# Performance work log

Hardware: AMD Instinct MI355X
Metric: run time of the kernel (lower is better)

Reference implementation:

```python
import jax, jax.numpy as jnp
import numpy as np
from jax import lax

STRIDE = (1, 1, 1, 1)
PADDING = (1, 1, 1, 1)
DILATION = (1, 1, 1, 1)


def setup_inputs() -> dict:
    key = jax.random.key(0)
    k1, k2, k3 = jax.random.split(key, 3)
    x = jax.random.normal(k1, (4, 32, 8, 24, 24, 24), dtype=jnp.float32)
    # weight layout matches torch ConvTranspose: (C_in, C_out, l_k, d_k, h_k, w_k)
    weight = jax.random.normal(k2, (32, 32, 3, 3, 3, 3), dtype=jnp.float32) * 0.05
    bias = jax.random.normal(k3, (32,), dtype=jnp.float32) * 0.05
    return {"x": x, "weight": weight, "bias": bias}


def _conv_transpose_4d(x, weight):
    # Transposed conv == conv with lhs dilated by stride, kernel spatially
    # flipped, and padding d*(k-1) - p on each side of each spatial dim.
    # Output size per dim: (i-1)*s - 2p + d*(k-1) + 1, identical to the
    # torch module's looped ConvTranspose3d + temporal scatter-add.
    ksp = weight.shape[2:]
    pads = [(d * (k - 1) - p, d * (k - 1) - p)
            for k, p, d in zip(ksp, PADDING, DILATION)]
    w = jnp.flip(weight, axis=(2, 3, 4, 5))  # (C_in, C_out, l, d, h, w)
    return lax.conv_general_dilated(
        x, w,
        window_strides=(1, 1, 1, 1),
        padding=pads,
        lhs_dilation=STRIDE,
        rhs_dilation=DILATION,
        dimension_numbers=("NCLDHW", "IOLDHW", "NCLDHW"),
    )


def reference(x, weight, bias):
    out = _conv_transpose_4d(x, weight)
    return out + bias.reshape(1, -1, 1, 1, 1, 1)
```

## Files before the change

### kernel.cpp

```cpp
#include <hip/hip_runtime.h>

#define NN 4
#define CC 32
#define LL 8
#define DD 24
#define HH 24
#define WW 24

typedef short  bf16x8  __attribute__((ext_vector_type(8)));
typedef float  f32x16  __attribute__((ext_vector_type(16)));
typedef unsigned short ushort8 __attribute__((ext_vector_type(8)));

#define XP_CHUNKS 2249728
#define XP_ELEMS  (XP_CHUNKS * 8)
#define AG_ELEMS  82944

__device__ __forceinline__ unsigned short f2bf(float f) {
    union { float f; unsigned u; } v; v.f = f;
    unsigned r = v.u + 0x7FFFu + ((v.u >> 16) & 1u);
    return (unsigned short)(r >> 16);
}

__device__ __forceinline__ void gload16(const void* g, void* l) {
    __builtin_amdgcn_global_load_lds(
        (const __attribute__((address_space(1))) unsigned int*)g,
        (__attribute__((address_space(3))) unsigned int*)l, 16, 0, 0);
}

__global__ __launch_bounds__(256) void prep(const float* __restrict__ x,
                                            const float* __restrict__ wgt,
                                            unsigned short* __restrict__ xp,
                                            unsigned short* __restrict__ Ag) {
    const int id = blockIdx.x * 256 + threadIdx.x;
    if (id < XP_CHUNKS) {
        const int wp = id % 26;
        const int r  = id / 26;
        const int g  = r & 1;
        const int r2 = r >> 1;
        const int hp = r2 % 26;
        const int slab = r2 / 26;
        const int dp = slab % 26;
        const int s2 = slab / 26;
        const int l  = s2 & 7;
        const int n  = (s2 >> 3) & 3;
        const int cig = s2 >> 5;
        const int dx = dp - 1, hx = hp - 1, wx = wp - 1;
        ushort8 v = {0, 0, 0, 0, 0, 0, 0, 0};
        if ((unsigned)dx < DD && (unsigned)hx < HH && (unsigned)wx < WW) {
            const int ci0 = cig * 16 + g * 8;
            const float* src = x + ((((size_t)n * CC + ci0) * LL + l) * DD + dx) * (HH * WW)
                             + hx * WW + wx;
#pragma unroll
            for (int ci = 0; ci < 8; ++ci)
                v[ci] = f2bf(src[(size_t)ci * (LL * DD * HH * WW)]);
        }
        const size_t dstc = ((size_t)r2 * 26 + wp) * 2 + g;
        *reinterpret_cast<ushort8*>(xp + dstc * 8) = v;
    } else {
        const int i = id - XP_CHUNKS;
        if (i < AG_ELEMS) {
            const int j  = i & 7;
            const int ln = (i >> 3) & 63;
            const int rest = i >> 9;
            const int s  = rest % 9;
            const int r  = rest / 9;
            const int qd = r % 3;
            const int ql = (r / 3) % 3;
            const int cig = r / 9;
            const int co = ln & 31, gg = ln >> 5;
            const int ci = cig * 16 + gg * 8 + j;
            const int tap = ql * 27 + qd * 9 + s;
            Ag[i] = f2bf(wgt[((size_t)ci * CC + co) * 81 + 80 - tap]);
        }
    }
}

__global__ __launch_bounds__(384, 3) void convt4d_main(
    const unsigned short* __restrict__ xp, const unsigned short* __restrict__ Ag,
    const float* __restrict__ bias, float* __restrict__ out)
{
    __shared__ __align__(16) unsigned short xs[2][1378 * 8];
    __shared__ __align__(16) unsigned short As[2][576 * 8];

    int bid = (int)blockIdx.x;
    bid = (bid & 7) * 96 + (bid >> 3);
    const int n = bid / (LL * DD);
    const int l = (bid / DD) % LL;
    const int d = bid % DD;

    const int t    = (int)threadIdx.x;
    const int lane = t & 63;
    const int wave = t >> 6;
    const int g    = lane >> 5;
    const int dh   = (lane >> 3) & 3;
    const int dw   = lane & 7;
    const int h0   = wave * 4;

    const int ql0 = (l == 0) ? 1 : 0;
    const int nql = 3 - (l == 0) - (l == 7);
    const int nst = 6 * nql;

    f32x16 acc[3];
#pragma unroll
    for (int i = 0; i < 3; ++i)
#pragma unroll
        for (int j = 0; j < 16; ++j) acc[i][j] = 0.f;

    const int eb = ((h0 + dh) * 53 + dw * 2 + g) * 8;

    auto issue = [&](int st, int buf) {
        const int qd  = st % 3;
        const int r   = st / 3;
        const int ql  = ql0 + r % nql;
        const int cig = r / nql;
        const int lx  = l + ql - 1;
        const unsigned short* base =
            xp + (size_t)((((cig * 4 + n) * 8 + lx) * 26) + (d + qd)) * (676 * 16);
        unsigned short* dst = xs[buf];
#pragma unroll
        for (int k = 0; k < 4; ++k) {
            const int v = t + k * 384;
            if (k < 3 || v < 1378) {
                int row = v / 53;
                int su  = v - row;
                if (su > 1351) su = 1351;
                gload16(base + (size_t)su * 8, (char*)dst + (size_t)v * 16);
            }
        }
        const unsigned short* asrc = Ag + (size_t)((cig * 9 + ql * 3 + qd)) * 4608;
        gload16(asrc + (size_t)t * 8, (char*)As[buf] + (size_t)t * 16);
        if (t < 192)
            gload16(asrc + (size_t)(t + 384) * 8, (char*)As[buf] + (size_t)(t + 384) * 16);
    };

    issue(0, 0);

#pragma unroll 1
    for (int st = 0; st < nst; ++st) {
        const int buf = st & 1;
        __syncthreads();
        if (st + 1 < nst) issue(st + 1, buf ^ 1);

        const unsigned short* xb = xs[buf] + eb;
#pragma unroll
        for (int s = 0; s < 9; ++s) {
            bf16x8 a = *reinterpret_cast<const bf16x8*>(&As[buf][(s * 64 + lane) * 8]);
            const int qh = s / 3, qw = s % 3;
            const int o = (qh * 53 + qw * 2) * 8;
#pragma unroll
            for (int nt = 0; nt < 3; ++nt) {
                bf16x8 b = *reinterpret_cast<const bf16x8*>(xb + o + nt * 128);
                acc[nt] = __builtin_amdgcn_mfma_f32_32x32x16_bf16(a, b, acc[nt], 0, 0, 0);
            }
        }
    }

#pragma unroll
    for (int r = 0; r < 16; ++r) {
        const int co = (r & 3) + 8 * (r >> 2) + 4 * g;
        const float bv = bias[co];
        size_t ob = (((((size_t)n * CC + co) * LL + l) * DD + d) * HH + (h0 + dh)) * WW + dw;
        out[ob]      = acc[0][r] + bv;
        out[ob + 8]  = acc[1][r] + bv;
        out[ob + 16] = acc[2][r] + bv;
    }
}

extern "C" void kernel_launch(void* const* d_in, const int* in_sizes, int n_in,
                              void* d_out, int out_size, void* d_ws, size_t ws_size,
                              hipStream_t stream) {
    const float* x    = (const float*)d_in[0];
    const float* wgt  = (const float*)d_in[1];
    const float* bias = (const float*)d_in[2];
    float* out = (float*)d_out;

    unsigned short* xp = (unsigned short*)d_ws;
    unsigned short* Ag = xp + XP_ELEMS;

    prep<<<(XP_CHUNKS + AG_ELEMS) / 256, 256, 0, stream>>>(x, wgt, xp, Ag);
    convt4d_main<<<NN * LL * DD, 384, 0, stream>>>(xp, Ag, bias, out);
}
```

Before: 113.8 us.

## Compute two output depth slices per block to reuse input planes across qd taps

Each block now produces two adjacent d outputs over half the h range, with 192 threads. Every loaded input depth plane feeds both outputs' accumulators, which cuts redundant x-plane loads from three per output to two. Weights move to a triple-buffered ring keyed by tap. This doubles accumulator registers and drops the occupancy hint, which risks fewer resident waves and more complex scheduling.

```diff
diff --git a/kernel.cpp b/kernel.cpp
--- a/kernel.cpp
+++ b/kernel.cpp
@@ -75,18 +75,23 @@
     }
 }
 
-__global__ __launch_bounds__(384, 3) void convt4d_main(
+__global__ __launch_bounds__(192) void convt4d_main(
     const unsigned short* __restrict__ xp, const unsigned short* __restrict__ Ag,
     const float* __restrict__ bias, float* __restrict__ out)
 {
-    __shared__ __align__(16) unsigned short xs[2][1378 * 8];
-    __shared__ __align__(16) unsigned short As[2][576 * 8];
+    __shared__ __align__(16) unsigned short xs[2][742 * 8];
+    __shared__ __align__(16) unsigned short As[3][576 * 8];
 
     int bid = (int)blockIdx.x;
     bid = (bid & 7) * 96 + (bid >> 3);
-    const int n = bid / (LL * DD);
-    const int l = (bid / DD) % LL;
-    const int d = bid % DD;
+    const int hh = bid & 1;
+    const int r0 = bid >> 1;
+    const int pd = r0 % 12;
+    const int r1 = r0 / 12;
+    const int l  = r1 & 7;
+    const int n  = r1 >> 3;
+    const int d0 = pd * 2;
+    const int hb = hh * 12;
 
     const int t    = (int)threadIdx.x;
     const int lane = t & 63;
@@ -94,63 +99,111 @@
     const int g    = lane >> 5;
     const int dh   = (lane >> 3) & 3;
     const int dw   = lane & 7;
-    const int h0   = wave * 4;
 
     const int ql0 = (l == 0) ? 1 : 0;
     const int nql = 3 - (l == 0) - (l == 7);
-    const int nst = 6 * nql;
-
-    f32x16 acc[3];
-#pragma unroll
-    for (int i = 0; i < 3; ++i)
-#pragma unroll
-        for (int j = 0; j < 16; ++j) acc[i][j] = 0.f;
-
-    const int eb = ((h0 + dh) * 53 + dw * 2 + g) * 8;
-
-    auto issue = [&](int st, int buf) {
-        const int qd  = st % 3;
-        const int r   = st / 3;
+    const int nst = 8 * nql;
+    const int nq  = 6 * nql;
+
+    f32x16 acc[2][3];
+#pragma unroll
+    for (int o = 0; o < 2; ++o)
+#pragma unroll
+        for (int i = 0; i < 3; ++i)
+#pragma unroll
+            for (int j = 0; j < 16; ++j) acc[o][i][j] = 0.f;
+
+    const int eb = ((wave * 4 + dh) * 53 + dw * 2 + g) * 8;
+
+    auto issueX = [&](int st, int buf) {
+        const int p   = st & 3;
+        const int r   = st >> 2;
         const int ql  = ql0 + r % nql;
         const int cig = r / nql;
         const int lx  = l + ql - 1;
-        const unsigned short* base =
-            xp + (size_t)((((cig * 4 + n) * 8 + lx) * 26) + (d + qd)) * (676 * 16);
+        const int dpad = d0 + p;
+        const size_t base = ((size_t)(((cig * 4 + n) * 8 + lx) * 26) + dpad) * 1352
+                          + (size_t)hb * 52;
         unsigned short* dst = xs[buf];
 #pragma unroll
         for (int k = 0; k < 4; ++k) {
-            const int v = t + k * 384;
-            if (k < 3 || v < 1378) {
+            const int v = t + k * 192;
+            if (k < 3 || v < 742) {
                 int row = v / 53;
                 int su  = v - row;
-                if (su > 1351) su = 1351;
-                gload16(base + (size_t)su * 8, (char*)dst + (size_t)v * 16);
-            }
-        }
-        const unsigned short* asrc = Ag + (size_t)((cig * 9 + ql * 3 + qd)) * 4608;
-        gload16(asrc + (size_t)t * 8, (char*)As[buf] + (size_t)t * 16);
-        if (t < 192)
-            gload16(asrc + (size_t)(t + 384) * 8, (char*)As[buf] + (size_t)(t + 384) * 16);
+                if (su > 727) su = 727;
+                gload16(xp + (base + su) * 8, (char*)dst + (size_t)v * 16);
+            }
+        }
     };
-
-    issue(0, 0);
+    auto issueA = [&](int q) {
+        const int grp = q / 3, qd = q % 3;
+        const int ql  = ql0 + grp % nql;
+        const int cig = grp / nql;
+        const unsigned short* src = Ag + (size_t)(cig * 9 + ql * 3 + qd) * 4608;
+        unsigned short* dst = As[q % 3];
+        gload16(src + (size_t)t * 8,         (char*)dst + (size_t)t * 16);
+        gload16(src + (size_t)(t + 192) * 8, (char*)dst + (size_t)(t + 192) * 16);
+        gload16(src + (size_t)(t + 384) * 8, (char*)dst + (size_t)(t + 384) * 16);
+    };
+
+    issueX(0, 0);
+    issueA(0);
 
 #pragma unroll 1
     for (int st = 0; st < nst; ++st) {
         const int buf = st & 1;
+        const int p   = st & 3;
+        const int grp = st >> 2;
         __syncthreads();
-        if (st + 1 < nst) issue(st + 1, buf ^ 1);
+        if (st + 1 < nst) issueX(st + 1, buf ^ 1);
+        {
+            const int qn = 3 * grp + p + 1;
+            if (p < 3 && qn < nq) issueA(qn);
+        }
 
         const unsigned short* xb = xs[buf] + eb;
-#pragma unroll
-        for (int s = 0; s < 9; ++s) {
-            bf16x8 a = *reinterpret_cast<const bf16x8*>(&As[buf][(s * 64 + lane) * 8]);
-            const int qh = s / 3, qw = s % 3;
-            const int o = (qh * 53 + qw * 2) * 8;
-#pragma unroll
-            for (int nt = 0; nt < 3; ++nt) {
-                bf16x8 b = *reinterpret_cast<const bf16x8*>(xb + o + nt * 128);
-                acc[nt] = __builtin_amdgcn_mfma_f32_32x32x16_bf16(a, b, acc[nt], 0, 0, 0);
+        if (p == 0) {
+            const unsigned short* a0b = &As[0][lane * 8];
+#pragma unroll
+            for (int s = 0; s < 9; ++s) {
+                bf16x8 a0 = *reinterpret_cast<const bf16x8*>(a0b + s * 512);
+                const int qh = s / 3, qw = s % 3;
+                const int o = (qh * 53 + qw * 2) * 8;
+#pragma unroll
+                for (int nt = 0; nt < 3; ++nt) {
+                    bf16x8 b = *reinterpret_cast<const bf16x8*>(xb + o + nt * 128);
+                    acc[0][nt] = __builtin_amdgcn_mfma_f32_32x32x16_bf16(a0, b, acc[0][nt], 0, 0, 0);
+                }
+            }
+        } else if (p == 3) {
+            const unsigned short* a1b = &As[2][lane * 8];
+#pragma unroll
+            for (int s = 0; s < 9; ++s) {
+                bf16x8 a1 = *reinterpret_cast<const bf16x8*>(a1b + s * 512);
+                const int qh = s / 3, qw = s % 3;
+                const int o = (qh * 53 + qw * 2) * 8;
+#pragma unroll
+                for (int nt = 0; nt < 3; ++nt) {
+                    bf16x8 b = *reinterpret_cast<const bf16x8*>(xb + o + nt * 128);
+                    acc[1][nt] = __builtin_amdgcn_mfma_f32_32x32x16_bf16(a1, b, acc[1][nt], 0, 0, 0);
+                }
+            }
+        } else {
+            const unsigned short* a0b = &As[p][lane * 8];
+            const unsigned short* a1b = &As[p - 1][lane * 8];
+#pragma unroll
+            for (int s = 0; s < 9; ++s) {
+                bf16x8 a0 = *reinterpret_cast<const bf16x8*>(a0b + s * 512);
+                bf16x8 a1 = *reinterpret_cast<const bf16x8*>(a1b + s * 512);
+                const int qh = s / 3, qw = s % 3;
+                const int o = (qh * 53 + qw * 2) * 8;
+#pragma unroll
+                for (int nt = 0; nt < 3; ++nt) {
+                    bf16x8 b = *reinterpret_cast<const bf16x8*>(xb + o + nt * 128);
+                    acc[0][nt] = __builtin_amdgcn_mfma_f32_32x32x16_bf16(a0, b, acc[0][nt], 0, 0, 0);
+                    acc[1][nt] = __builtin_amdgcn_mfma_f32_32x32x16_bf16(a1, b, acc[1][nt], 0, 0, 0);
+                }
             }
         }
     }
@@ -159,10 +212,14 @@
     for (int r = 0; r < 16; ++r) {
         const int co = (r & 3) + 8 * (r >> 2) + 4 * g;
         const float bv = bias[co];
-        size_t ob = (((((size_t)n * CC + co) * LL + l) * DD + d) * HH + (h0 + dh)) * WW + dw;
-        out[ob]      = acc[0][r] + bv;
-        out[ob + 8]  = acc[1][r] + bv;
-        out[ob + 16] = acc[2][r] + bv;
+#pragma unroll
+        for (int o = 0; o < 2; ++o) {
+            size_t ob = (((((size_t)n * CC + co) * LL + l) * DD + (d0 + o)) * HH
+                       + (hb + wave * 4 + dh)) * WW + dw;
+            out[ob]      = acc[o][0][r] + bv;
+            out[ob + 8]  = acc[o][1][r] + bv;
+            out[ob + 16] = acc[o][2][r] + bv;
+        }
     }
 }
 
@@ -178,5 +235,5 @@
     unsigned short* Ag = xp + XP_ELEMS;
 
     prep<<<(XP_CHUNKS + AG_ELEMS) / 256, 256, 0, stream>>>(x, wgt, xp, Ag);
-    convt4d_main<<<NN * LL * DD, 384, 0, stream>>>(xp, Ag, bias, out);
-}
+    convt4d_main<<<768, 192, 0, stream>>>(xp, Ag, bias, out);
+}
```

New measurement: 141.9 us. 24.7% more time.
